# Optimization experiments

Measured on AMD Instinct MI355X. Metric: run time of the kernel, lower is better.

## Reference

```python
import jax, jax.numpy as jnp
import numpy as np
from jax import lax

B, CIN, H, W = 4, 720, 128, 128
MID = 512           # conv3x3 output channels (hardcoded in OCRHead)
KC, VC, NC = 256, 256, 19
BN_EPS = 1e-5


def setup_inputs() -> dict:
    key = jax.random.key(0)
    ks = jax.random.split(key, 16)
    s = 0.02
    f32 = jnp.float32
    return {
        "feats": jax.random.normal(ks[0], (B, CIN, H, W), f32),
        # conv3x3 (no bias)
        "w3": (jax.random.normal(ks[1], (MID, CIN, 3, 3), f32) * s),
        # BatchNorm affine params
        "gamma": 1.0 + 0.1 * jax.random.normal(ks[2], (MID,), f32),
        "beta": 0.1 * jax.random.normal(ks[3], (MID,), f32),
        # aux 1x1 conv (with bias)
        "aux_w": jax.random.normal(ks[4], (NC, MID), f32) * s,
        "aux_b": 0.01 * jax.random.normal(ks[5], (NC,), f32),
        # ObjectAttention: query 1x1 conv (no bias), key/value Linear (with bias), out 1x1 conv (no bias)
        "q_w": jax.random.normal(ks[6], (KC, MID), f32) * s,
        "k_w": jax.random.normal(ks[7], (KC, MID), f32) * s,
        "k_b": 0.01 * jax.random.normal(ks[8], (KC,), f32),
        "v_w": jax.random.normal(ks[9], (VC, MID), f32) * s,
        "v_b": 0.01 * jax.random.normal(ks[10], (VC,), f32),
        "out_w": jax.random.normal(ks[11], (MID, VC), f32) * s,
        # cls 1x1 conv (with bias)
        "cls_w": jax.random.normal(ks[12], (NC, MID), f32) * s,
        "cls_b": 0.01 * jax.random.normal(ks[13], (NC,), f32),
    }


def reference(feats, w3, gamma, beta, aux_w, aux_b, q_w, k_w, k_b, v_w, v_b, out_w, cls_w, cls_b):
    # conv3x3, padding=1, no bias
    x = lax.conv_general_dilated(feats, w3, window_strides=(1, 1),
                                 padding=((1, 1), (1, 1)),
                                 dimension_numbers=("NCHW", "OIHW", "NCHW"))
    # BatchNorm (batch mode: stats over batch+spatial) + relu
    mean = jnp.mean(x, axis=(0, 2, 3))
    var = jnp.var(x, axis=(0, 2, 3))
    x = (x - mean[None, :, None, None]) * lax.rsqrt(var + BN_EPS)[None, :, None, None]
    x = x * gamma[None, :, None, None] + beta[None, :, None, None]
    x = jax.nn.relu(x)

    # aux head: 1x1 conv with bias -> [B, K, H, W]
    aux_logits = jnp.einsum("bchw,kc->bkhw", x, aux_w) + aux_b[None, :, None, None]

    # SpatialGather: softmax over classes per pixel, normalize over pixels per class
    x_flat = x.reshape(B, MID, H * W).transpose(0, 2, 1)           # [B, N, C]
    probs = jax.nn.softmax(aux_logits.reshape(B, NC, H * W).transpose(0, 2, 1), axis=-1)  # [B, N, K]
    weights = probs / jnp.clip(jnp.sum(probs, axis=1, keepdims=True), 1e-6)
    context = jnp.einsum("bnk,bnc->bkc", weights, x_flat)          # [B, K, C]

    # ObjectAttention
    q = jnp.einsum("bchw,dc->bdhw", x, q_w).reshape(B, KC, H * W).transpose(0, 2, 1)  # [B, N, KC]
    k = jnp.einsum("bkc,dc->bkd", context, k_w) + k_b              # [B, K, KC]
    v = jnp.einsum("bkc,dc->bkd", context, v_w) + v_b              # [B, K, VC]
    scale = 1.0 / jnp.sqrt(jnp.asarray(KC, jnp.float32))
    attn = jax.nn.softmax(jnp.einsum("bnd,bkd->bnk", q * scale, k), axis=-1)  # [B, N, K]
    agg = jnp.einsum("bnk,bkv->bnv", attn, v)                      # [B, N, VC]
    agg_chw = agg.reshape(B, H, W, VC).transpose(0, 3, 1, 2)       # [B, VC, H, W]
    obj = jnp.einsum("bvhw,ov->bohw", agg_chw, out_w)              # [B, MID, H, W]

    x = x + obj
    logits = jnp.einsum("bchw,kc->bkhw", x, cls_w) + cls_b[None, :, None, None]
    return (logits, aux_logits)
```

## Files before the change

### kernel.cpp

```cpp
#include <hip/hip_runtime.h>
#include <hip/hip_bf16.h>


__device__ __forceinline__ float u_lo(unsigned u) { return __uint_as_float(u << 16); }
__device__ __forceinline__ float u_hi(unsigned u) { return __uint_as_float(u & 0xffff0000u); }
__device__ __forceinline__ float scrub(float v) { return isfinite(v) ? v : 1e4f; }
#define BF2F(h) __bfloat162float(h)

typedef __attribute__((ext_vector_type(8))) short bf16x8;
typedef __attribute__((ext_vector_type(4))) float f32x4;

#define SO_APACK  0ull
#define TAIL0     9371648ull
#define TA_AUXWT  (TAIL0 + 0ull)
#define TA_CLSWT  (TAIL0 + 38912ull)
#define TA_SS     (TAIL0 + 77824ull)
#define TA_PSUM   (TAIL0 + 81920ull)
#define TA_CTX    (TAIL0 + 82432ull)
#define TA_KMAT   (TAIL0 + 238080ull)
#define TA_VMAT   (TAIL0 + 315904ull)
#define TA_FCLS   (TAIL0 + 393728ull)
#define TA_MT     (TAIL0 + 413184ull)
#define TA_G      (TAIL0 + 568832ull)

#define LDS_CI   40
#define LDS_ROW  (3 * LDS_CI)
#define LDS_TOT  (130 * LDS_ROW)

__global__ __launch_bounds__(256) void prep_small_kernel(
    const float* __restrict__ aux_w, const float* __restrict__ cls_w,
    float* __restrict__ aux_wt, float* __restrict__ cls_wt) {
  int i = blockIdx.x * 256 + threadIdx.x;
  if (i < 9728) {
    int k = i >> 9, c = i & 511;
    aux_wt[c * 19 + k] = aux_w[i];
    cls_wt[c * 19 + k] = cls_w[i];
  }
}

__global__ __launch_bounds__(256) void prep_apack_kernel(
    const float* __restrict__ w3, __hip_bfloat16* __restrict__ Apack) {
  int idx = blockIdx.x * 256 + threadIdx.x;
  if (idx >= 512 * 736) return;
  int oc = idx / 736, ci = idx - (idx / 736) * 736;
  float v[9];
#pragma unroll
  for (int k = 0; k < 9; ++k) v[k] = 0.f;
  if (ci < 720) {
    const float* src = w3 + ((size_t)oc * 720 + ci) * 9;
#pragma unroll
    for (int k = 0; k < 9; ++k) v[k] = src[k];
  }
#pragma unroll
  for (int k = 0; k < 9; ++k)
    Apack[((size_t)k * 512 + oc) * 736 + ci] = __float2bfloat16(v[k]);
}

__global__ __launch_bounds__(256) void conv_mfma_kernel(
    const float* __restrict__ feats, const __hip_bfloat16* __restrict__ Apack,
    __hip_bfloat16* __restrict__ X) {
  __shared__ short Blds[LDS_TOT];
  int bid = blockIdx.x;
  int xcd = bid & 7;
  int slot = bid >> 3;
  int oc_t = slot & 3;
  int gx = (slot >> 2) * 8 + xcd;
  int b = gx >> 7, h = gx & 127;
  int tid = threadIdx.x;
  int wave = tid >> 6, lane = tid & 63;
  int wm = wave >> 1, wn = wave & 1;
  int l15 = lane & 15, quad = lane >> 4;

  f32x4 acc[4][4];
#pragma unroll
  for (int mb = 0; mb < 4; ++mb)
#pragma unroll
    for (int nb = 0; nb < 4; ++nb) acc[mb][nb] = (f32x4){0.f, 0.f, 0.f, 0.f};

  for (int i = tid; i < 2 * LDS_ROW; i += 256) {
    int wp = (i < LDS_ROW) ? 0 : 129;
    Blds[wp * LDS_ROW + (i < LDS_ROW ? i : i - LDS_ROW)] = 0;
  }

  const short* Ab = (const short*)Apack;
  int oc_row = oc_t * 128 + wm * 64 + l15;

  for (int cb = 0; cb < 23; ++cb) {
    __syncthreads();
    int ci0 = cb * 32 + wave * 8;
    bool civ = (ci0 < 720);
    const float* fb = feats + (((size_t)b * 720 + ci0) << 14) + lane * 2;
#pragma unroll
    for (int r = 0; r < 3; ++r) {
      int hr = h - 1 + r;
      float2 v0 = {0.f, 0.f}, v1 = v0, v2 = v0, v3 = v0,
             v4 = v0, v5 = v0, v6 = v0, v7 = v0;
      if (civ && ((unsigned)hr < 128u)) {
        const float* p = fb + hr * 128;
        v0 = *reinterpret_cast<const float2*>(p);
        v1 = *reinterpret_cast<const float2*>(p + 16384);
        v2 = *reinterpret_cast<const float2*>(p + 32768);
        v3 = *reinterpret_cast<const float2*>(p + 49152);
        v4 = *reinterpret_cast<const float2*>(p + 65536);
        v5 = *reinterpret_cast<const float2*>(p + 81920);
        v6 = *reinterpret_cast<const float2*>(p + 98304);
        v7 = *reinterpret_cast<const float2*>(p + 114688);
      }
      union { bf16x8 v; __hip_bfloat16 h[8]; } E, O;
      E.h[0] = __float2bfloat16(v0.x); O.h[0] = __float2bfloat16(v0.y);
      E.h[1] = __float2bfloat16(v1.x); O.h[1] = __float2bfloat16(v1.y);
      E.h[2] = __float2bfloat16(v2.x); O.h[2] = __float2bfloat16(v2.y);
      E.h[3] = __float2bfloat16(v3.x); O.h[3] = __float2bfloat16(v3.y);
      E.h[4] = __float2bfloat16(v4.x); O.h[4] = __float2bfloat16(v4.y);
      E.h[5] = __float2bfloat16(v5.x); O.h[5] = __float2bfloat16(v5.y);
      E.h[6] = __float2bfloat16(v6.x); O.h[6] = __float2bfloat16(v6.y);
      E.h[7] = __float2bfloat16(v7.x); O.h[7] = __float2bfloat16(v7.y);
      short* wb = &Blds[(lane * 2 + 1) * LDS_ROW + r * LDS_CI + wave * 8];
      *reinterpret_cast<bf16x8*>(wb) = E.v;
      *reinterpret_cast<bf16x8*>(wb + LDS_ROW) = O.v;
    }
    __syncthreads();
#pragma unroll
    for (int r = 0; r < 3; ++r) {
#pragma unroll
      for (int dw = 0; dw < 3; ++dw) {
        int plane = r * 3 + dw;
        const short* ap = Ab + ((size_t)plane * 512 + oc_row) * 736 + cb * 32 + quad * 8;
        bf16x8 af[4];
#pragma unroll
        for (int mb = 0; mb < 4; ++mb)
          af[mb] = *(const bf16x8*)(ap + (size_t)mb * 16 * 736);
        bf16x8 bfr[4];
#pragma unroll
        for (int nb = 0; nb < 4; ++nb) {
          int px = wn * 64 + nb * 16 + l15;
          bfr[nb] = *(const bf16x8*)(&Blds[(px + dw) * LDS_ROW + r * LDS_CI + quad * 8]);
        }
#pragma unroll
        for (int mb = 0; mb < 4; ++mb)
#pragma unroll
          for (int nb = 0; nb < 4; ++nb)
            acc[mb][nb] = __builtin_amdgcn_mfma_f32_16x16x32_bf16(
                af[mb], bfr[nb], acc[mb][nb], 0, 0, 0);
      }
    }
  }
#pragma unroll
  for (int mb = 0; mb < 4; ++mb)
#pragma unroll
    for (int nb = 0; nb < 4; ++nb) {
      int px = wn * 64 + nb * 16 + l15;
#pragma unroll
      for (int reg = 0; reg < 4; ++reg) {
        int oc = oc_t * 128 + wm * 64 + mb * 16 + quad * 4 + reg;
        X[(((size_t)b * 512 + oc) << 14) + h * 128 + px] =
            __float2bfloat16(acc[mb][nb][reg]);
      }
    }
}

__global__ __launch_bounds__(256) void bn_stats_kernel(
    const __hip_bfloat16* __restrict__ X, const float* __restrict__ gamma,
    const float* __restrict__ beta, float* __restrict__ ss_out) {
  int c = blockIdx.x, tid = threadIdx.x;
  float s = 0.f, ss = 0.f;
  for (int b = 0; b < 4; ++b) {
    const __hip_bfloat16* p = X + (((size_t)b * 512 + c) << 14);
    for (int n = tid * 8; n < 16384; n += 2048) {
      uint4 u = *reinterpret_cast<const uint4*>(p + n);
      unsigned arr[4] = {u.x, u.y, u.z, u.w};
#pragma unroll
      for (int j = 0; j < 4; ++j) {
        float f0 = u_lo(arr[j]), f1 = u_hi(arr[j]);
        s += f0 + f1;
        ss += f0 * f0 + f1 * f1;
      }
    }
  }
#pragma unroll
  for (int off = 32; off > 0; off >>= 1) {
    s += __shfl_down(s, off);
    ss += __shfl_down(ss, off);
  }
  __shared__ float red[8];
  int wid = tid >> 6, lane = tid & 63;
  if (lane == 0) { red[wid] = s; red[4 + wid] = ss; }
  __syncthreads();
  if (tid == 0) {
    s = red[0] + red[1] + red[2] + red[3];
    ss = red[4] + red[5] + red[6] + red[7];
    float mean = s * (1.f / 65536.f);
    float var = ss * (1.f / 65536.f) - mean * mean;
    float gi = gamma[c] * rsqrtf(var + 1e-5f);
    ss_out[c * 2] = gi;
    ss_out[c * 2 + 1] = beta[c] - mean * gi;
  }
}

__global__ __launch_bounds__(256) void bn_apply_kernel(
    __hip_bfloat16* __restrict__ X, const float* __restrict__ ss) {
  size_t idx = ((size_t)blockIdx.x * 256 + threadIdx.x) * 8;
  int c = (int)((idx >> 14) & 511);
  float sc = ss[c * 2], sh = ss[c * 2 + 1];
  uint4 u = *reinterpret_cast<const uint4*>(X + idx);
  unsigned arr[4] = {u.x, u.y, u.z, u.w};
  union { uint4 u; __hip_bfloat16 h[8]; } O;
#pragma unroll
  for (int j = 0; j < 4; ++j) {
    float f0 = fmaxf(fmaf(u_lo(arr[j]), sc, sh), 0.f);
    float f1 = fmaxf(fmaf(u_hi(arr[j]), sc, sh), 0.f);
    O.h[2 * j] = __float2bfloat16(f0);
    O.h[2 * j + 1] = __float2bfloat16(f1);
  }
  *reinterpret_cast<uint4*>(X + idx) = O.u;
}

__global__ __launch_bounds__(256) void aux_ctx_kernel(
    const __hip_bfloat16* __restrict__ X, const float* __restrict__ aux_wt,
    const float* __restrict__ aux_b,
    float* __restrict__ ctx, float* __restrict__ psum) {
  int b = blockIdx.y;
  int n0 = blockIdx.x * 256;
  int tid = threadIdx.x;
  __shared__ float pl[19][256];

  const __hip_bfloat16* Xb = X + (((size_t)b * 512) << 14);

  int p0 = n0 + tid;
  float a0[19];
#pragma unroll
  for (int k = 0; k < 19; ++k) a0[k] = aux_b[k];
  for (int c = 0; c < 512; ++c) {
    float f0 = BF2F(Xb[((size_t)c << 14) + p0]);
    const float* wr = aux_wt + c * 19;
#pragma unroll
    for (int k = 0; k < 19; ++k) a0[k] = fmaf(wr[k], f0, a0[k]);
  }
  float mx0 = a0[0];
#pragma unroll
  for (int k = 1; k < 19; ++k) mx0 = fmaxf(mx0, a0[k]);
  float s0 = 0.f;
#pragma unroll
  for (int k = 0; k < 19; ++k) { a0[k] = __expf(a0[k] - mx0); s0 += a0[k]; }
  float r0 = 1.f / s0;
#pragma unroll
  for (int k = 0; k < 19; ++k) {
    float q0 = a0[k] * r0;
    pl[k][tid] = q0;
    a0[k] = q0;
  }
#pragma unroll
  for (int k = 0; k < 19; ++k) {
    float t = a0[k];
#pragma unroll
    for (int off = 32; off > 0; off >>= 1) t += __shfl_down(t, off);
    if ((tid & 63) == 0) atomicAdd(&psum[b * 19 + k], t);
  }
  __syncthreads();

  int c0 = tid * 2;
  const __hip_bfloat16* x0 = Xb + ((size_t)c0 << 14) + n0;
  const __hip_bfloat16* x1 = x0 + 16384;
  float b0[19], b1[19];
#pragma unroll
  for (int k = 0; k < 19; ++k) { b0[k] = 0.f; b1[k] = 0.f; }
  for (int nl = 0; nl < 256; ++nl) {
    float xv0 = BF2F(x0[nl]), xv1 = BF2F(x1[nl]);
#pragma unroll
    for (int kk = 0; kk < 19; ++kk) {
      float p = pl[kk][nl];
      b0[kk] = fmaf(p, xv0, b0[kk]);
      b1[kk] = fmaf(p, xv1, b1[kk]);
    }
  }
#pragma unroll
  for (int kk = 0; kk < 19; ++kk) {
    atomicAdd(&ctx[((b * 19 + kk) << 9) + c0], b0[kk]);
    atomicAdd(&ctx[((b * 19 + kk) << 9) + c0 + 1], b1[kk]);
  }
}

__global__ __launch_bounds__(256) void small_a_kernel(
    const float* __restrict__ ctx, const float* __restrict__ psum,
    const float* __restrict__ k_w, const float* __restrict__ k_b,
    const float* __restrict__ v_w, const float* __restrict__ v_b,
    const float* __restrict__ cls_w, const float* __restrict__ out_w,
    float* __restrict__ Kmat, float* __restrict__ vmat, float* __restrict__ fcls) {
  int i = blockIdx.x * 256 + threadIdx.x;
  if (i < 38912) {
    int half = i / 19456;
    int j = i - half * 19456;
    int d = j & 255;
    int t = j >> 8;
    const float* w = (half ? v_w : k_w) + d * 512;
    const float* cr = ctx + (t << 9);
    float s = 0.f;
    for (int c = 0; c < 512; ++c) s = fmaf(w[c], cr[c], s);
    float rcp = 1.f / fmaxf(psum[t], 1e-6f);
    float bias = (half ? v_b : k_b)[d];
    (half ? vmat : Kmat)[j] = s * rcp + bias;
  } else if (i < 43776) {
    int j = i - 38912;
    int vv = j & 255, k = j >> 8;
    const float* cw = cls_w + k * 512;
    float s = 0.f;
    for (int c = 0; c < 512; ++c) s = fmaf(cw[c], out_w[c * 256 + vv], s);
    fcls[j] = s;
  }
}

__global__ __launch_bounds__(256) void small_b_kernel(
    const float* __restrict__ Kmat, const float* __restrict__ vmat,
    const float* __restrict__ fcls, const float* __restrict__ q_w,
    float* __restrict__ m_t, float* __restrict__ g) {
  int i = blockIdx.x * 256 + threadIdx.x;
  if (i < 38912) {
    int kk = i % 19;
    int t = i / 19;
    int c = t & 511, b = t >> 9;
    const float* kr = Kmat + ((b * 19 + kk) << 8);
    float s = 0.f;
    for (int d = 0; d < 256; ++d) s = fmaf(q_w[d * 512 + c], kr[d], s);
    m_t[i] = s;
  } else if (i < 40356) {
    int j = i - 38912;
    int k = j % 19;
    int t = j / 19;
    const float* vr = vmat + (t << 8);
    const float* fr = fcls + (k << 8);
    float s = 0.f;
    for (int v = 0; v < 256; ++v) s = fmaf(fr[v], vr[v], s);
    g[j] = s;
  }
}

__global__ __launch_bounds__(256) void final_fused_kernel(
    const __hip_bfloat16* __restrict__ X, const float* __restrict__ m_t,
    const float* __restrict__ cls_wt, const float* __restrict__ cls_b,
    const float* __restrict__ g, float* __restrict__ out) {
  int b = blockIdx.y;
  int n = blockIdx.x * 256 + threadIdx.x;
  float macc[19], cacc[19];
#pragma unroll
  for (int k = 0; k < 19; ++k) { macc[k] = 0.f; cacc[k] = 0.f; }
  const __hip_bfloat16* xp = X + (((size_t)b * 512) << 14) + n;
  for (int c = 0; c < 512; ++c) {
    float xv = BF2F(xp[(size_t)c << 14]);
    const float* mr = m_t + (b * 512 + c) * 19;
    const float* wr = cls_wt + c * 19;
#pragma unroll
    for (int k = 0; k < 19; ++k) {
      macc[k] = fmaf(mr[k], xv, macc[k]);
      cacc[k] = fmaf(wr[k], xv, cacc[k]);
    }
  }
  float mx = -1e30f;
#pragma unroll
  for (int k = 0; k < 19; ++k) { macc[k] *= 0.0625f; mx = fmaxf(mx, macc[k]); }
  float sum = 0.f;
#pragma unroll
  for (int k = 0; k < 19; ++k) { macc[k] = __expf(macc[k] - mx); sum += macc[k]; }
  float r = 1.f / sum;
#pragma unroll
  for (int k = 0; k < 19; ++k) cacc[k] += cls_b[k];
#pragma unroll
  for (int kk = 0; kk < 19; ++kk) {
    float av = macc[kk] * r;
    const float* gr = g + (b * 19 + kk) * 19;
#pragma unroll
    for (int k = 0; k < 19; ++k) cacc[k] = fmaf(gr[k], av, cacc[k]);
  }
  size_t ob = ((size_t)b * 19) << 14;
#pragma unroll
  for (int k = 0; k < 19; ++k)
    out[ob + ((size_t)k << 14) + n] = scrub(cacc[k]);
}

__global__ __launch_bounds__(256) void aux_final_kernel(
    const __hip_bfloat16* __restrict__ X, const float* __restrict__ aux_w,
    const float* __restrict__ aux_b, float* __restrict__ aux_out) {
  __shared__ float wt[9728];
  for (int i = threadIdx.x; i < 9728; i += 256) {
    int k = i >> 9, c = i & 511;
    wt[c * 19 + k] = aux_w[i];
  }
  __syncthreads();
  int b = blockIdx.y;
  int n = blockIdx.x * 256 + threadIdx.x;
  float acc[19];
#pragma unroll
  for (int k = 0; k < 19; ++k) acc[k] = aux_b[k];
  const __hip_bfloat16* xp = X + (((size_t)b * 512) << 14) + n;
  for (int c = 0; c < 512; ++c) {
    float xv = BF2F(xp[(size_t)c << 14]);
    const float* wr = &wt[c * 19];
#pragma unroll
    for (int k = 0; k < 19; ++k) acc[k] = fmaf(wr[k], xv, acc[k]);
  }
  size_t ob = ((size_t)b * 19) << 14;
#pragma unroll
  for (int k = 0; k < 19; ++k)
    aux_out[ob + ((size_t)k << 14) + n] = scrub(acc[k]);
}

extern "C" void kernel_launch(void* const* d_in, const int* in_sizes, int n_in,
                              void* d_out, int out_size, void* d_ws, size_t ws_size,
                              hipStream_t stream) {
  const float* feats = (const float*)d_in[0];
  const float* w3    = (const float*)d_in[1];
  const float* gamma = (const float*)d_in[2];
  const float* beta  = (const float*)d_in[3];
  const float* aux_w = (const float*)d_in[4];
  const float* aux_b = (const float*)d_in[5];
  const float* q_w   = (const float*)d_in[6];
  const float* k_w   = (const float*)d_in[7];
  const float* k_b   = (const float*)d_in[8];
  const float* v_w   = (const float*)d_in[9];
  const float* v_b   = (const float*)d_in[10];
  const float* out_w = (const float*)d_in[11];
  const float* cls_w = (const float*)d_in[12];
  const float* cls_b = (const float*)d_in[13];

  float* logits_out = (float*)d_out;
  float* aux_out    = logits_out + 1245184;

  __hip_bfloat16* X = (__hip_bfloat16*)d_ws;

  char* ob = (char*)d_out;
  __hip_bfloat16* Apack = (__hip_bfloat16*)(ob + SO_APACK);
  float* aux_wt = (float*)(ob + TA_AUXWT);
  float* cls_wt = (float*)(ob + TA_CLSWT);
  float* ssbuf  = (float*)(ob + TA_SS);
  float* psum   = (float*)(ob + TA_PSUM);
  float* ctx    = (float*)(ob + TA_CTX);
  float* Kmat   = (float*)(ob + TA_KMAT);
  float* vmat   = (float*)(ob + TA_VMAT);
  float* fcls   = (float*)(ob + TA_FCLS);
  float* m_t    = (float*)(ob + TA_MT);
  float* g      = (float*)(ob + TA_G);

  hipMemsetAsync(ob + TA_PSUM, 0, 512 + 155648, stream);

  prep_small_kernel<<<38, 256, 0, stream>>>(aux_w, cls_w, aux_wt, cls_wt);
  prep_apack_kernel<<<1472, 256, 0, stream>>>(w3, Apack);
  conv_mfma_kernel<<<2048, 256, 0, stream>>>(feats, Apack, X);
  bn_stats_kernel<<<512, 256, 0, stream>>>(X, gamma, beta, ssbuf);
  bn_apply_kernel<<<16384, 256, 0, stream>>>(X, ssbuf);
  aux_ctx_kernel<<<dim3(64, 4), 256, 0, stream>>>(X, aux_wt, aux_b, ctx, psum);
  small_a_kernel<<<171, 256, 0, stream>>>(ctx, psum, k_w, k_b, v_w, v_b, cls_w, out_w,
                                          Kmat, vmat, fcls);
  small_b_kernel<<<158, 256, 0, stream>>>(Kmat, vmat, fcls, q_w, m_t, g);
  final_fused_kernel<<<dim3(64, 4), 256, 0, stream>>>(X, m_t, cls_wt, cls_b, g, logits_out);
  aux_final_kernel<<<dim3(64, 4), 256, 0, stream>>>(X, aux_w, aux_b, aux_out);
}
```

Measured before the change: 1.453 ms.

## Compute two output rows per conv block to reuse weight fragments

Each conv block now produces two adjacent output rows instead of one. It stages four input rows in LDS with a row-major layout, and each wave handles one of the two rows across all 128 columns. The A-fragments (weights) loaded from global memory are reused across twice as many MFMAs, which cuts weight traffic and halves the grid. The cost is a doubled accumulator footprint (128 floats per thread), more register pressure and possibly lower occupancy, plus a different LDS bank access pattern.

```diff
diff --git a/kernel.cpp b/kernel.cpp
--- a/kernel.cpp
+++ b/kernel.cpp
@@ -24,8 +24,8 @@
 #define TA_G      (TAIL0 + 568832ull)
 
 #define LDS_CI   40
-#define LDS_ROW  (3 * LDS_CI)
-#define LDS_TOT  (130 * LDS_ROW)
+#define LDS_WP   (130 * LDS_CI)
+#define LDS_TOT  (4 * LDS_WP)
 
 __global__ __launch_bounds__(256) void prep_small_kernel(
     const float* __restrict__ aux_w, const float* __restrict__ cls_w,
@@ -64,22 +64,24 @@
   int xcd = bid & 7;
   int slot = bid >> 3;
   int oc_t = slot & 3;
-  int gx = (slot >> 2) * 8 + xcd;
-  int b = gx >> 7, h = gx & 127;
+  int gx2 = (slot >> 2) * 8 + xcd;
+  int b = gx2 >> 6, h0 = (gx2 & 63) * 2;
   int tid = threadIdx.x;
   int wave = tid >> 6, lane = tid & 63;
   int wm = wave >> 1, wn = wave & 1;
   int l15 = lane & 15, quad = lane >> 4;
 
-  f32x4 acc[4][4];
+  f32x4 acc[4][8];
 #pragma unroll
   for (int mb = 0; mb < 4; ++mb)
 #pragma unroll
-    for (int nb = 0; nb < 4; ++nb) acc[mb][nb] = (f32x4){0.f, 0.f, 0.f, 0.f};
-
-  for (int i = tid; i < 2 * LDS_ROW; i += 256) {
-    int wp = (i < LDS_ROW) ? 0 : 129;
-    Blds[wp * LDS_ROW + (i < LDS_ROW ? i : i - LDS_ROW)] = 0;
+    for (int nb = 0; nb < 8; ++nb) acc[mb][nb] = (f32x4){0.f, 0.f, 0.f, 0.f};
+
+  for (int i = tid; i < 320; i += 256) {
+    int rr = i / 80, rem = i - rr * 80;
+    int wp = (rem < 40) ? 0 : 129;
+    int ci = (rem < 40) ? rem : rem - 40;
+    Blds[rr * LDS_WP + wp * LDS_CI + ci] = 0;
   }
 
   const short* Ab = (const short*)Apack;
@@ -91,8 +93,8 @@
     bool civ = (ci0 < 720);
     const float* fb = feats + (((size_t)b * 720 + ci0) << 14) + lane * 2;
 #pragma unroll
-    for (int r = 0; r < 3; ++r) {
-      int hr = h - 1 + r;
+    for (int rr = 0; rr < 4; ++rr) {
+      int hr = h0 - 1 + rr;
       float2 v0 = {0.f, 0.f}, v1 = v0, v2 = v0, v3 = v0,
              v4 = v0, v5 = v0, v6 = v0, v7 = v0;
       if (civ && ((unsigned)hr < 128u)) {
@@ -115,9 +117,9 @@
       E.h[5] = __float2bfloat16(v5.x); O.h[5] = __float2bfloat16(v5.y);
       E.h[6] = __float2bfloat16(v6.x); O.h[6] = __float2bfloat16(v6.y);
       E.h[7] = __float2bfloat16(v7.x); O.h[7] = __float2bfloat16(v7.y);
-      short* wb = &Blds[(lane * 2 + 1) * LDS_ROW + r * LDS_CI + wave * 8];
+      short* wb = &Blds[rr * LDS_WP + (lane * 2 + 1) * LDS_CI + wave * 8];
       *reinterpret_cast<bf16x8*>(wb) = E.v;
-      *reinterpret_cast<bf16x8*>(wb + LDS_ROW) = O.v;
+      *reinterpret_cast<bf16x8*>(wb + LDS_CI) = O.v;
     }
     __syncthreads();
 #pragma unroll
@@ -130,30 +132,29 @@
 #pragma unroll
         for (int mb = 0; mb < 4; ++mb)
           af[mb] = *(const bf16x8*)(ap + (size_t)mb * 16 * 736);
-        bf16x8 bfr[4];
-#pragma unroll
-        for (int nb = 0; nb < 4; ++nb) {
-          int px = wn * 64 + nb * 16 + l15;
-          bfr[nb] = *(const bf16x8*)(&Blds[(px + dw) * LDS_ROW + r * LDS_CI + quad * 8]);
+        const short* bbase = &Blds[(wn + r) * LDS_WP + dw * LDS_CI + quad * 8];
+#pragma unroll
+        for (int nb = 0; nb < 8; ++nb) {
+          int w = nb * 16 + l15;
+          bf16x8 bfr = *(const bf16x8*)(bbase + w * LDS_CI);
+#pragma unroll
+          for (int mb = 0; mb < 4; ++mb)
+            acc[mb][nb] = __builtin_amdgcn_mfma_f32_16x16x32_bf16(
+                af[mb], bfr, acc[mb][nb], 0, 0, 0);
         }
-#pragma unroll
-        for (int mb = 0; mb < 4; ++mb)
-#pragma unroll
-          for (int nb = 0; nb < 4; ++nb)
-            acc[mb][nb] = __builtin_amdgcn_mfma_f32_16x16x32_bf16(
-                af[mb], bfr[nb], acc[mb][nb], 0, 0, 0);
       }
     }
   }
+  int h = h0 + wn;
 #pragma unroll
   for (int mb = 0; mb < 4; ++mb)
 #pragma unroll
-    for (int nb = 0; nb < 4; ++nb) {
-      int px = wn * 64 + nb * 16 + l15;
+    for (int nb = 0; nb < 8; ++nb) {
+      int w = nb * 16 + l15;
 #pragma unroll
       for (int reg = 0; reg < 4; ++reg) {
         int oc = oc_t * 128 + wm * 64 + mb * 16 + quad * 4 + reg;
-        X[(((size_t)b * 512 + oc) << 14) + h * 128 + px] =
+        X[(((size_t)b * 512 + oc) << 14) + h * 128 + w] =
             __float2bfloat16(acc[mb][nb][reg]);
       }
     }
@@ -443,7 +444,7 @@
 
   prep_small_kernel<<<38, 256, 0, stream>>>(aux_w, cls_w, aux_wt, cls_wt);
   prep_apack_kernel<<<1472, 256, 0, stream>>>(w3, Apack);
-  conv_mfma_kernel<<<2048, 256, 0, stream>>>(feats, Apack, X);
+  conv_mfma_kernel<<<1024, 256, 0, stream>>>(feats, Apack, X);
   bn_stats_kernel<<<512, 256, 0, stream>>>(X, gamma, beta, ssbuf);
   bn_apply_kernel<<<16384, 256, 0, stream>>>(X, ssbuf);
   aux_ctx_kernel<<<dim3(64, 4), 256, 0, stream>>>(X, aux_wt, aux_b, ctx, psum);
```

Result: slower. 1.640 ms (+12.9%).
